# Optimization experiments

Measured on AMD Instinct MI355X. Metric: run time of the kernel, lower is better.

The kernel has to match this reference:

```python
import jax, jax.numpy as jnp
import numpy as np

B, N, L = 4, 64, 64
D_MODEL = 128
D_INNER = 256   # expand=2
D_STATE = 16
D_CONV = 4
DT_RANK = 8     # ceil(D_MODEL/16)
N_LAYERS = 4
EPS = 1e-5


def setup_inputs() -> dict:
    key = jax.random.key(0)
    ks = jax.random.split(key, 16)
    f = jnp.float32
    s = 0.05
    return {
        'mha_in': jax.random.normal(ks[0], (B, N, L, D_MODEL), f),
        'mamba_mask': jax.random.bernoulli(ks[1], 0.9, (B, N, L)),
        'mlp_w1': jax.random.normal(ks[2], (D_MODEL, D_MODEL), f) * s,
        'mlp_b1': jnp.zeros((D_MODEL,), f),
        'mlp_w2': jax.random.normal(ks[3], (D_MODEL, D_MODEL), f) * s,
        'mlp_b2': jnp.zeros((D_MODEL,), f),
        'in_proj_w': jax.random.normal(ks[4], (N_LAYERS, 2 * D_INNER, D_MODEL), f) * s,
        'conv_w': jax.random.normal(ks[5], (N_LAYERS, D_INNER, D_CONV), f) * s,
        'conv_b': jnp.zeros((N_LAYERS, D_INNER), f),
        'x_proj_w': jax.random.normal(ks[6], (N_LAYERS, DT_RANK + 2 * D_STATE, D_INNER), f) * s,
        'dt_proj_w': jax.random.normal(ks[7], (N_LAYERS, D_INNER, DT_RANK), f) * s,
        'dt_proj_b': jax.random.uniform(ks[8], (N_LAYERS, D_INNER), f, -4.0, -2.0),
        'A_log': jnp.log(jnp.broadcast_to(jnp.arange(1, D_STATE + 1, dtype=f), (N_LAYERS, D_INNER, D_STATE))),
        'D_skip': jnp.ones((N_LAYERS, D_INNER), f),
        'out_proj_w': jax.random.normal(ks[9], (N_LAYERS, D_MODEL, D_INNER), f) * s,
        'blk_norm_w': jnp.ones((N_LAYERS, D_MODEL), f),
        'norm_f_w': jnp.ones((D_MODEL,), f),
    }


def rmsnorm(x, w):
    # fused add-RMSNorm keeps residual in fp32; weight multiply after normalize
    x32 = x.astype(jnp.float32)
    return (x32 * jax.lax.rsqrt(jnp.mean(x32 * x32, -1, keepdims=True) + EPS)) * w


def causal_conv1d(x, w, b):
    # x: [R, L, d_inner]; depthwise causal conv (torch conv1d, padding=D_CONV-1, truncated to L)
    xp = jnp.pad(x, ((0, 0), (D_CONV - 1, 0), (0, 0)))
    y = jnp.zeros_like(x) + b
    for k in range(D_CONV):
        y = y + w[:, k] * xp[:, k:k + L, :]
    return y


def selective_scan(u, dt, A, Bm, Cm, D_sk):
    # u, dt: [R, L, d_inner]; A: [d_inner, n]; Bm, Cm: [R, L, n]
    def step(h, inputs):
        dt_t, B_t, C_t, u_t = inputs  # [R,di], [R,n], [R,n], [R,di]
        dA = jnp.exp(dt_t[..., None] * A)                       # [R,di,n]
        h = dA * h + (dt_t * u_t)[..., None] * B_t[:, None, :]  # [R,di,n]
        y = jnp.einsum('rdn,rn->rd', h, C_t)
        return h, y
    h0 = jnp.zeros((u.shape[0], A.shape[0], A.shape[1]), u.dtype)
    xs = (dt.swapaxes(0, 1), Bm.swapaxes(0, 1), Cm.swapaxes(0, 1), u.swapaxes(0, 1))
    _, ys = jax.lax.scan(step, h0, xs)
    return ys.swapaxes(0, 1) + u * D_sk


def mamba_mixer(x, in_w, conv_w, conv_b, xproj_w, dt_w, dt_b, A_log, D_sk, out_w):
    xz = x @ in_w.T                             # [R,L,2*d_inner]
    xc, z = jnp.split(xz, 2, axis=-1)
    xc = jax.nn.silu(causal_conv1d(xc, conv_w, conv_b))
    x_dbl = xc @ xproj_w.T                      # [R,L,dt_rank+2n]
    dt = jax.nn.softplus(x_dbl[..., :DT_RANK] @ dt_w.T + dt_b)
    Bm = x_dbl[..., DT_RANK:DT_RANK + D_STATE]
    Cm = x_dbl[..., DT_RANK + D_STATE:]
    A = -jnp.exp(A_log)
    y = selective_scan(xc, dt, A, Bm, Cm, D_sk)
    return (y * jax.nn.silu(z)) @ out_w.T


def _forward(mha_in, mamba_mask, mlp_w1, mlp_b1, mlp_w2, mlp_b2, in_proj_w, conv_w,
             conv_b, x_proj_w, dt_proj_w, dt_proj_b, A_log, D_skip, out_proj_w,
             blk_norm_w, norm_f_w):
    R = B * N
    x = mha_in.reshape(R, L, D_MODEL)
    key_valid = jnp.any(mamba_mask.reshape(R, L), axis=-1)
    # hist_embed_mlp: Linear -> GELU(exact) -> Linear
    h = jax.nn.gelu(x @ mlp_w1.T + mlp_b1, approximate=False) @ mlp_w2.T + mlp_b2
    residual = None
    for i in range(N_LAYERS):
        residual = h if residual is None else h + residual  # fused add (fp32 residual)
        hn = rmsnorm(residual, blk_norm_w[i])
        h = mamba_mixer(hn, in_proj_w[i], conv_w[i], conv_b[i], x_proj_w[i],
                        dt_proj_w[i], dt_proj_b[i], A_log[i], D_skip[i], out_proj_w[i])
    residual = h + residual
    out = rmsnorm(residual, norm_f_w)            # prenorm=False final fused add-norm
    # scatter into zeros over valid rows == mask-multiply (rows independent)
    out = out * key_valid[:, None, None].astype(out.dtype)
    out = out.reshape(B, N, L, D_MODEL)
    return out[:, 0, -1, :]                      # ag_feat[:, -1, :]


def reference(mha_in, mamba_mask, mlp_w1, mlp_b1, mlp_w2, mlp_b2, in_proj_w, conv_w,
              conv_b, x_proj_w, dt_proj_w, dt_proj_b, A_log, D_skip, out_proj_w,
              blk_norm_w, norm_f_w):
    return _forward(mha_in, mamba_mask, mlp_w1, mlp_b1, mlp_w2, mlp_b2, in_proj_w,
                    conv_w, conv_b, x_proj_w, dt_proj_w, dt_proj_b, A_log, D_skip,
                    out_proj_w, blk_norm_w, norm_f_w)
```

## Files before the change

kernel.cpp:

```cpp
#include <hip/hip_runtime.h>
#include <math.h>

#define NWG  64
#define NTHR 512

#define WS_XG 512
#define WS_DT (WS_XG + 65536)
#define WS_DU (WS_DT + 65536)
#define WS_BC (WS_DU + 65536)
#define WS_Y  (WS_BC + 8192)

__device__ __forceinline__ float silu_f(float v) { return v / (1.0f + __expf(-v)); }
__device__ __forceinline__ float dot4(float4 a, float4 b) {
    return a.x*b.x + a.y*b.y + a.z*b.z + a.w*b.w;
}
__device__ __forceinline__ float wave_red_sum(float v) {
    v += __shfl_xor(v, 1);  v += __shfl_xor(v, 2);  v += __shfl_xor(v, 4);
    v += __shfl_xor(v, 8);  v += __shfl_xor(v, 16); v += __shfl_xor(v, 32);
    return v;
}
__device__ __forceinline__ float red8(float v) {
    v += __shfl_xor(v, 1);  v += __shfl_xor(v, 2);  v += __shfl_xor(v, 4);
    return v;
}
__device__ __forceinline__ float sel4(int ln, float a0, float a1, float a2, float a3) {
    return ln==0 ? a0 : (ln==1 ? a1 : (ln==2 ? a2 : a3));
}
__device__ __forceinline__ float aload(const float* p) {
    return __hip_atomic_load(p, __ATOMIC_RELAXED, __HIP_MEMORY_SCOPE_AGENT);
}
__device__ __forceinline__ void astore(float* p, float v) {
    __hip_atomic_store(p, v, __ATOMIC_RELAXED, __HIP_MEMORY_SCOPE_AGENT);
}

__device__ __forceinline__ void seq_barrier(unsigned* slot) {
    __syncthreads();
    if (threadIdx.x == 0) {
        asm volatile("s_waitcnt vmcnt(0)" ::: "memory");
        __hip_atomic_fetch_add(slot, 1u, __ATOMIC_RELAXED, __HIP_MEMORY_SCOPE_AGENT);
        while (__hip_atomic_load(slot, __ATOMIC_RELAXED, __HIP_MEMORY_SCOPE_AGENT) < 16u)
            __builtin_amdgcn_s_sleep(1);
    }
    __syncthreads();
}

__global__ __launch_bounds__(NTHR, 1) void fused_kernel(
    const float* __restrict__ mha_in, const int* __restrict__ mask,
    const float* __restrict__ mlp_w1, const float* __restrict__ mlp_b1,
    const float* __restrict__ mlp_w2, const float* __restrict__ mlp_b2,
    const float* __restrict__ in_proj_w, const float* __restrict__ conv_w,
    const float* __restrict__ conv_b, const float* __restrict__ x_proj_w,
    const float* __restrict__ dt_proj_w, const float* __restrict__ dt_proj_b,
    const float* __restrict__ A_log, const float* __restrict__ D_skip,
    const float* __restrict__ out_proj_w, const float* __restrict__ blk_norm_w,
    const float* __restrict__ norm_f_w,
    float* __restrict__ ws, float* __restrict__ out)
{
    const int wg = blockIdx.x;
    const int t  = threadIdx.x;
    const int s  = wg & 3;
    const int rb = wg >> 2;
    const int l0 = rb * 4;
    const int r0 = s*64 + l0;
    const int d0 = rb * 16;
    const int h  = t >> 7;
    const int c  = t & 127;
    const int wave = t >> 6;
    const int grp = t >> 3, ln = t & 7;

    unsigned* bar = (unsigned*)ws;
    float* xg  = ws + WS_XG;
    float* dtg = ws + WS_DT;
    float* dug = ws + WS_DU;
    float* bcg = ws + WS_BC;
    float* yg  = ws + WS_Y;

    __shared__ float bufX[4][256];
    __shared__ float bufZ[4][256];
    __shared__ float bufA[4][256];
    __shared__ float bufG[4][256];
    __shared__ float bufB[4][128];
    __shared__ float bufR[4][128];
    __shared__ float xdS[4][40];
    __shared__ float sdt[64][17];
    __shared__ float sdu[64][17];
    __shared__ float sbc[64][33];
    __shared__ float part[8];
    __shared__ int   anyv;

    float resid;

    float4 w1v[8], w2v[8];
    {
        #pragma unroll
        for (int pass = 0; pass < 2; ++pass) {
            const int j = pass*64 + grp;
            const float* w1p = mlp_w1 + (size_t)j*128 + ln*4;
            const float* w2p = mlp_w2 + (size_t)j*128 + ln*4;
            #pragma unroll
            for (int i = 0; i < 4; ++i) {
                w1v[pass*4+i] = *(const float4*)&w1p[i*32];
                w2v[pass*4+i] = *(const float4*)&w2p[i*32];
            }
        }
    }
    bufB[h][c] = mha_in[(size_t)s*524288 + (size_t)(l0 + h)*128 + c];
    __syncthreads();
    {
        #pragma unroll
        for (int pass = 0; pass < 2; ++pass) {
            const int j = pass*64 + grp;
            float a0=0.f, a1=0.f, a2=0.f, a3=0.f;
            #pragma unroll
            for (int i = 0; i < 4; ++i) {
                float4 wv = w1v[pass*4+i];
                a0 += dot4(*(const float4*)&bufB[0][ln*4 + i*32], wv);
                a1 += dot4(*(const float4*)&bufB[1][ln*4 + i*32], wv);
                a2 += dot4(*(const float4*)&bufB[2][ln*4 + i*32], wv);
                a3 += dot4(*(const float4*)&bufB[3][ln*4 + i*32], wv);
            }
            a0 = red8(a0); a1 = red8(a1); a2 = red8(a2); a3 = red8(a3);
            if (ln < 4) {
                float v = sel4(ln, a0, a1, a2, a3) + mlp_b1[j];
                bufA[ln][j] = 0.5f*v*(1.0f + erff(v*0.70710678118f));
            }
        }
    }
    __syncthreads();
    {
        #pragma unroll
        for (int pass = 0; pass < 2; ++pass) {
            const int j = pass*64 + grp;
            float a0=0.f, a1=0.f, a2=0.f, a3=0.f;
            #pragma unroll
            for (int i = 0; i < 4; ++i) {
                float4 wv = w2v[pass*4+i];
                a0 += dot4(*(const float4*)&bufA[0][ln*4 + i*32], wv);
                a1 += dot4(*(const float4*)&bufA[1][ln*4 + i*32], wv);
                a2 += dot4(*(const float4*)&bufA[2][ln*4 + i*32], wv);
                a3 += dot4(*(const float4*)&bufA[3][ln*4 + i*32], wv);
            }
            a0 = red8(a0); a1 = red8(a1); a2 = red8(a2); a3 = red8(a3);
            if (ln < 4)
                bufR[ln][j] = sel4(ln, a0, a1, a2, a3) + mlp_b2[j];
        }
    }
    __syncthreads();
    resid = bufR[h][c];
    __syncthreads();

    for (int layer = 0; layer < 4; ++layer) {
        unsigned* s1slot = bar + (layer*4 + s)*16;
        unsigned* s2slot = bar + 256 + layer*4 + s;
        unsigned* s3slot = bar + 272 + layer*4 + s;

        float4 wx[16];
        {
            #pragma unroll
            for (int pass = 0; pass < 4; ++pass) {
                const float* w = in_proj_w + ((size_t)layer*512 + pass*64 + grp)*128 + ln*4;
                #pragma unroll
                for (int i = 0; i < 4; ++i) wx[pass*4+i] = *(const float4*)&w[i*32];
            }
        }

        {
            float sq = wave_red_sum(resid*resid);
            if ((t & 63) == 0) part[wave] = sq;
        }
        __syncthreads();
        {
            float sr = part[h*2] + part[h*2 + 1];
            float sc = rsqrtf(sr*(1.0f/128.0f) + 1e-5f);
            bufB[h][c] = resid * sc * blk_norm_w[layer*128 + c];
        }
        __syncthreads();

        {
            #pragma unroll
            for (int pass = 0; pass < 4; ++pass) {
                const int j = pass*64 + grp;
                float a0=0.f, a1=0.f, a2=0.f, a3=0.f;
                #pragma unroll
                for (int i = 0; i < 4; ++i) {
                    float4 wv = wx[pass*4+i];
                    a0 += dot4(*(const float4*)&bufB[0][ln*4 + i*32], wv);
                    a1 += dot4(*(const float4*)&bufB[1][ln*4 + i*32], wv);
                    a2 += dot4(*(const float4*)&bufB[2][ln*4 + i*32], wv);
                    a3 += dot4(*(const float4*)&bufB[3][ln*4 + i*32], wv);
                }
                a0 = red8(a0); a1 = red8(a1); a2 = red8(a2); a3 = red8(a3);
                if (ln < 4) {
                    float v = sel4(ln, a0, a1, a2, a3);
                    bufX[ln][j] = v;
                    astore(&xg[(size_t)(r0 + ln)*256 + j], v);
                }
            }
        }
        __syncthreads();
        if (t == 0) {
            asm volatile("s_waitcnt vmcnt(0)" ::: "memory");
            __hip_atomic_fetch_add(s1slot + rb, 1u, __ATOMIC_RELAXED, __HIP_MEMORY_SCOPE_AGENT);
            if (rb > 0) {
                while (__hip_atomic_load(s1slot + rb - 1, __ATOMIC_RELAXED, __HIP_MEMORY_SCOPE_AGENT) == 0u)
                    __builtin_amdgcn_s_sleep(1);
            }
        }
        __syncthreads();

        float4 wxp[8];
        if (t < 320) {
            const float* xw = x_proj_w + ((size_t)layer*40 + grp)*256 + ln*4;
            #pragma unroll
            for (int i = 0; i < 8; ++i) wxp[i] = *(const float4*)&xw[i*32];
        }

        {
            int d = t & 255, half = t >> 8;
            int rbase = s*64;
            float4 cw = *(const float4*)&conv_w[((size_t)layer*256 + d)*4];
            float cb = conv_b[layer*256 + d];
            if (half == 0) {
                float x0 = (l0-3 >= 0) ? aload(&xg[(size_t)(rbase+l0-3)*256 + d]) : 0.f;
                float x1 = (l0-2 >= 0) ? aload(&xg[(size_t)(rbase+l0-2)*256 + d]) : 0.f;
                float x2 = (l0-1 >= 0) ? aload(&xg[(size_t)(rbase+l0-1)*256 + d]) : 0.f;
                float x3 = bufX[0][d];
                float x4 = bufX[1][d];
                bufA[0][d] = silu_f(cb + cw.x*x0 + cw.y*x1 + cw.z*x2 + cw.w*x3);
                bufA[1][d] = silu_f(cb + cw.x*x1 + cw.y*x2 + cw.z*x3 + cw.w*x4);
            } else {
                float x0 = (l0-1 >= 0) ? aload(&xg[(size_t)(rbase+l0-1)*256 + d]) : 0.f;
                float x1 = bufX[0][d];
                float x2 = bufX[1][d];
                float x3 = bufX[2][d];
                float x4 = bufX[3][d];
                bufA[2][d] = silu_f(cb + cw.x*x0 + cw.y*x1 + cw.z*x2 + cw.w*x3);
                bufA[3][d] = silu_f(cb + cw.x*x1 + cw.y*x2 + cw.z*x3 + cw.w*x4);
            }
        }
        __syncthreads();

        if (t < 320) {
            const int jx = grp;
            float a0=0.f, a1=0.f, a2=0.f, a3=0.f;
            #pragma unroll
            for (int i = 0; i < 8; ++i) {
                float4 wv = wxp[i];
                a0 += dot4(*(const float4*)&bufA[0][ln*4 + i*32], wv);
                a1 += dot4(*(const float4*)&bufA[1][ln*4 + i*32], wv);
                a2 += dot4(*(const float4*)&bufA[2][ln*4 + i*32], wv);
                a3 += dot4(*(const float4*)&bufA[3][ln*4 + i*32], wv);
            }
            a0 = red8(a0); a1 = red8(a1); a2 = red8(a2); a3 = red8(a3);
            if (ln < 4) {
                float v = sel4(ln, a0, a1, a2, a3);
                xdS[ln][jx] = v;
                if (jx >= 8)
                    astore(&bcg[(size_t)(r0+ln)*32 + (jx-8)], v);
            }
        }
        __syncthreads();

        {
            int d = t & 255, half = t >> 8;
            const float* dw = dt_proj_w + ((size_t)layer*256 + d)*8;
            float4 wa = *(const float4*)&dw[0];
            float4 wb = *(const float4*)&dw[4];
            float b = dt_proj_b[layer*256 + d];
            #pragma unroll
            for (int q = 0; q < 2; ++q) {
                int rloc = half*2 + q;
                float4 xa = *(const float4*)&xdS[rloc][0];
                float4 xb = *(const float4*)&xdS[rloc][4];
                float pre = b + dot4(xa, wa) + dot4(xb, wb);
                float sp = (pre > 20.f) ? pre : log1pf(__expf(pre));
                astore(&dtg[(size_t)(r0+rloc)*256 + d], sp);
                astore(&dug[(size_t)(r0+rloc)*256 + d], sp * bufA[rloc][d]);
            }
        }
        seq_barrier(s2slot);

        if (t < 256) {
            int l = t >> 2, q = t & 3;
            const float* p = &dtg[(size_t)(s*64+l)*256 + d0 + q*4];
            sdt[l][q*4]   = aload(p);     sdt[l][q*4+1] = aload(p+1);
            sdt[l][q*4+2] = aload(p+2);   sdt[l][q*4+3] = aload(p+3);
        } else {
            int tt = t - 256; int l = tt >> 2, q = tt & 3;
            const float* p = &dug[(size_t)(s*64+l)*256 + d0 + q*4];
            sdu[l][q*4]   = aload(p);     sdu[l][q*4+1] = aload(p+1);
            sdu[l][q*4+2] = aload(p+2);   sdu[l][q*4+3] = aload(p+3);
        }
        {
            int l = t >> 3, q = t & 7;
            const float* p = &bcg[(size_t)(s*64+l)*32 + q*4];
            sbc[l][q*4]   = aload(p);     sbc[l][q*4+1] = aload(p+1);
            sbc[l][q*4+2] = aload(p+2);   sbc[l][q*4+3] = aload(p+3);
        }
        __syncthreads();

        if (t < 64) {
            const int dloc = t >> 2, sub = t & 3, d = d0 + dloc;
            const float* Ab = A_log + ((size_t)layer*256 + d)*16 + sub*4;
            float A0 = -__expf(Ab[0]), A1 = -__expf(Ab[1]);
            float A2 = -__expf(Ab[2]), A3 = -__expf(Ab[3]);
            float h0 = 0.f, h1v = 0.f, h2v = 0.f, h3v = 0.f;
            #pragma unroll 4
            for (int l = 0; l < 64; ++l) {
                float dtv = sdt[l][dloc];
                float duv = sdu[l][dloc];
                float4 B4, C4;
                B4.x = sbc[l][sub*4];      B4.y = sbc[l][sub*4+1];
                B4.z = sbc[l][sub*4+2];    B4.w = sbc[l][sub*4+3];
                C4.x = sbc[l][16+sub*4];   C4.y = sbc[l][16+sub*4+1];
                C4.z = sbc[l][16+sub*4+2]; C4.w = sbc[l][16+sub*4+3];
                float dA, yp;
                dA = __expf(dtv*A0); h0  = dA*h0  + duv*B4.x; yp  = h0 *C4.x;
                dA = __expf(dtv*A1); h1v = dA*h1v + duv*B4.y; yp += h1v*C4.y;
                dA = __expf(dtv*A2); h2v = dA*h2v + duv*B4.z; yp += h2v*C4.z;
                dA = __expf(dtv*A3); h3v = dA*h3v + duv*B4.w; yp += h3v*C4.w;
                yp += __shfl_xor(yp, 1);
                yp += __shfl_xor(yp, 2);
                if (sub == 0) astore(&yg[(size_t)(s*64+l)*256 + d], yp);
            }
        } else if (t >= 256) {
            const int tz = t - 256, gz = tz >> 3, lz = tz & 7;
            #pragma unroll
            for (int halfb = 0; halfb < 2; ++halfb) {
                float4 wv[16];
                #pragma unroll
                for (int pass = 0; pass < 4; ++pass) {
                    const int j = (halfb*4 + pass)*32 + gz;
                    const float* w = in_proj_w + ((size_t)layer*512 + 256 + j)*128 + lz*4;
                    #pragma unroll
                    for (int i = 0; i < 4; ++i) wv[pass*4+i] = *(const float4*)&w[i*32];
                }
                #pragma unroll
                for (int pass = 0; pass < 4; ++pass) {
                    const int j = (halfb*4 + pass)*32 + gz;
                    float a0=0.f, a1=0.f, a2=0.f, a3=0.f;
                    #pragma unroll
                    for (int i = 0; i < 4; ++i) {
                        float4 w4 = wv[pass*4+i];
                        a0 += dot4(*(const float4*)&bufB[0][lz*4 + i*32], w4);
                        a1 += dot4(*(const float4*)&bufB[1][lz*4 + i*32], w4);
                        a2 += dot4(*(const float4*)&bufB[2][lz*4 + i*32], w4);
                        a3 += dot4(*(const float4*)&bufB[3][lz*4 + i*32], w4);
                    }
                    a0 += __shfl_xor(a0, 1); a0 += __shfl_xor(a0, 2); a0 += __shfl_xor(a0, 4);
                    a1 += __shfl_xor(a1, 1); a1 += __shfl_xor(a1, 2); a1 += __shfl_xor(a1, 4);
                    a2 += __shfl_xor(a2, 1); a2 += __shfl_xor(a2, 2); a2 += __shfl_xor(a2, 4);
                    a3 += __shfl_xor(a3, 1); a3 += __shfl_xor(a3, 2); a3 += __shfl_xor(a3, 4);
                    if (lz < 4)
                        bufZ[lz][j] = sel4(lz, a0, a1, a2, a3);
                }
            }
        }
        seq_barrier(s3slot);

        float4 wo[16];
        {
            #pragma unroll
            for (int pass = 0; pass < 2; ++pass) {
                const float* w = out_proj_w + ((size_t)layer*128 + pass*64 + grp)*256 + ln*4;
                #pragma unroll
                for (int i = 0; i < 8; ++i) wo[pass*8+i] = *(const float4*)&w[i*32];
            }
        }

        {
            int d = t & 255, half = t >> 8;
            float Dsk = D_skip[layer*256 + d];
            #pragma unroll
            for (int q = 0; q < 2; ++q) {
                int rloc = half*2 + q; int r = r0 + rloc;
                float z = bufZ[rloc][d];
                float yv = aload(&yg[(size_t)r*256 + d]) + bufA[rloc][d]*Dsk;
                bufG[rloc][d] = yv * silu_f(z);
            }
        }
        __syncthreads();

        {
            #pragma unroll
            for (int pass = 0; pass < 2; ++pass) {
                const int j = pass*64 + grp;
                float a0=0.f, a1=0.f, a2=0.f, a3=0.f;
                #pragma unroll
                for (int i = 0; i < 8; ++i) {
                    float4 wv = wo[pass*8+i];
                    a0 += dot4(*(const float4*)&bufG[0][ln*4 + i*32], wv);
                    a1 += dot4(*(const float4*)&bufG[1][ln*4 + i*32], wv);
                    a2 += dot4(*(const float4*)&bufG[2][ln*4 + i*32], wv);
                    a3 += dot4(*(const float4*)&bufG[3][ln*4 + i*32], wv);
                }
                a0 = red8(a0); a1 = red8(a1); a2 = red8(a2); a3 = red8(a3);
                if (ln < 4)
                    bufR[ln][j] = sel4(ln, a0, a1, a2, a3);
            }
        }
        __syncthreads();
        resid += bufR[h][c];
        __syncthreads();
    }

    if (t == 0) anyv = 0;
    __syncthreads();
    if (rb == 15) {
        if (t < 64 && mask[s*4096 + t] != 0) anyv = 1;
        float sq = wave_red_sum(resid*resid);
        if ((t & 63) == 0) part[wave] = sq;
    }
    __syncthreads();
    if (rb == 15 && h == 3) {
        float sr = part[6] + part[7];
        float sc = rsqrtf(sr*(1.0f/128.0f) + 1e-5f);
        float o  = resid * sc * norm_f_w[c];
        out[s*128 + c] = anyv ? o : 0.f;
    }
}

extern "C" void kernel_launch(void* const* d_in, const int* in_sizes, int n_in,
                              void* d_out, int out_size, void* d_ws, size_t ws_size,
                              hipStream_t stream) {
    (void)in_sizes; (void)n_in; (void)out_size; (void)ws_size;
    const float* mha_in     = (const float*)d_in[0];
    const int*   mask       = (const int*)  d_in[1];
    const float* mlp_w1     = (const float*)d_in[2];
    const float* mlp_b1     = (const float*)d_in[3];
    const float* mlp_w2     = (const float*)d_in[4];
    const float* mlp_b2     = (const float*)d_in[5];
    const float* in_proj_w  = (const float*)d_in[6];
    const float* conv_w     = (const float*)d_in[7];
    const float* conv_b     = (const float*)d_in[8];
    const float* x_proj_w   = (const float*)d_in[9];
    const float* dt_proj_w  = (const float*)d_in[10];
    const float* dt_proj_b  = (const float*)d_in[11];
    const float* A_log      = (const float*)d_in[12];
    const float* D_skip     = (const float*)d_in[13];
    const float* out_proj_w = (const float*)d_in[14];
    const float* blk_norm_w = (const float*)d_in[15];
    const float* norm_f_w   = (const float*)d_in[16];
    float* ws  = (float*)d_ws;
    float* out = (float*)d_out;

    hipMemsetAsync(d_ws, 0, 2048, stream);

    fused_kernel<<<NWG, NTHR, 0, stream>>>(
        mha_in, mask, mlp_w1, mlp_b1, mlp_w2, mlp_b2,
        in_proj_w, conv_w, conv_b, x_proj_w, dt_proj_w, dt_proj_b,
        A_log, D_skip, out_proj_w, blk_norm_w, norm_f_w, ws, out);
}
```

Baseline: 205.2 us.

## Spread selective scan over four waves and prefetch next layer's in_proj weights

The selective scan now runs on 256 threads, one state element per lane, with a 16-lane shuffle reduction, instead of 64 threads each handling four states serially. This shortens the serial dependency chain of the scan recurrence. The next layer's in_proj weights are loaded into registers during the current layer's out_proj phase, so global load latency overlaps with compute. The cost is higher register pressure (a second 16-float4 buffer) and more shuffles per step.

```diff
diff --git a/kernel.cpp b/kernel.cpp
--- a/kernel.cpp
+++ b/kernel.cpp
@@ -149,20 +149,20 @@
     resid = bufR[h][c];
     __syncthreads();
 
+    float4 wx[16];
+    {
+        #pragma unroll
+        for (int pass = 0; pass < 4; ++pass) {
+            const float* w = in_proj_w + ((size_t)pass*64 + grp)*128 + ln*4;
+            #pragma unroll
+            for (int i = 0; i < 4; ++i) wx[pass*4+i] = *(const float4*)&w[i*32];
+        }
+    }
+
     for (int layer = 0; layer < 4; ++layer) {
         unsigned* s1slot = bar + (layer*4 + s)*16;
         unsigned* s2slot = bar + 256 + layer*4 + s;
         unsigned* s3slot = bar + 272 + layer*4 + s;
-
-        float4 wx[16];
-        {
-            #pragma unroll
-            for (int pass = 0; pass < 4; ++pass) {
-                const float* w = in_proj_w + ((size_t)layer*512 + pass*64 + grp)*128 + ln*4;
-                #pragma unroll
-                for (int i = 0; i < 4; ++i) wx[pass*4+i] = *(const float4*)&w[i*32];
-            }
-        }
 
         {
             float sq = wave_red_sum(resid*resid);
@@ -299,31 +299,29 @@
         }
         __syncthreads();
 
-        if (t < 64) {
-            const int dloc = t >> 2, sub = t & 3, d = d0 + dloc;
-            const float* Ab = A_log + ((size_t)layer*256 + d)*16 + sub*4;
-            float A0 = -__expf(Ab[0]), A1 = -__expf(Ab[1]);
-            float A2 = -__expf(Ab[2]), A3 = -__expf(Ab[3]);
-            float h0 = 0.f, h1v = 0.f, h2v = 0.f, h3v = 0.f;
+        if (t < 256) {
+            const int lane = t & 63, w4 = t >> 6;
+            const int cl = lane >> 4, n = lane & 15;
+            const int lch = w4*4 + cl;
+            const int d = d0 + lch;
+            const float A = -__expf(A_log[((size_t)(layer*256 + d))*16 + n]);
+            float hst = 0.f;
             #pragma unroll 4
             for (int l = 0; l < 64; ++l) {
-                float dtv = sdt[l][dloc];
-                float duv = sdu[l][dloc];
-                float4 B4, C4;
-                B4.x = sbc[l][sub*4];      B4.y = sbc[l][sub*4+1];
-                B4.z = sbc[l][sub*4+2];    B4.w = sbc[l][sub*4+3];
-                C4.x = sbc[l][16+sub*4];   C4.y = sbc[l][16+sub*4+1];
-                C4.z = sbc[l][16+sub*4+2]; C4.w = sbc[l][16+sub*4+3];
-                float dA, yp;
-                dA = __expf(dtv*A0); h0  = dA*h0  + duv*B4.x; yp  = h0 *C4.x;
-                dA = __expf(dtv*A1); h1v = dA*h1v + duv*B4.y; yp += h1v*C4.y;
-                dA = __expf(dtv*A2); h2v = dA*h2v + duv*B4.z; yp += h2v*C4.z;
-                dA = __expf(dtv*A3); h3v = dA*h3v + duv*B4.w; yp += h3v*C4.w;
-                yp += __shfl_xor(yp, 1);
-                yp += __shfl_xor(yp, 2);
-                if (sub == 0) astore(&yg[(size_t)(s*64+l)*256 + d], yp);
-            }
-        } else if (t >= 256) {
+                float dtv = sdt[l][lch];
+                float duv = sdu[l][lch];
+                float Bn  = sbc[l][n];
+                float Cn  = sbc[l][16 + n];
+                float dA  = __expf(dtv * A);
+                hst = dA*hst + duv*Bn;
+                float p = hst * Cn;
+                p += __shfl_xor(p, 1);
+                p += __shfl_xor(p, 2);
+                p += __shfl_xor(p, 4);
+                p += __shfl_xor(p, 8);
+                if (n == 0) astore(&yg[(size_t)(s*64+l)*256 + d], p);
+            }
+        } else {
             const int tz = t - 256, gz = tz >> 3, lz = tz & 7;
             #pragma unroll
             for (int halfb = 0; halfb < 2; ++halfb) {
@@ -367,6 +365,15 @@
                 for (int i = 0; i < 8; ++i) wo[pass*8+i] = *(const float4*)&w[i*32];
             }
         }
+        float4 wxn[16];
+        if (layer < 3) {
+            #pragma unroll
+            for (int pass = 0; pass < 4; ++pass) {
+                const float* w = in_proj_w + ((size_t)(layer+1)*512 + pass*64 + grp)*128 + ln*4;
+                #pragma unroll
+                for (int i = 0; i < 4; ++i) wxn[pass*4+i] = *(const float4*)&w[i*32];
+            }
+        }
 
         {
             int d = t & 255, half = t >> 8;
@@ -402,6 +409,11 @@
         __syncthreads();
         resid += bufR[h][c];
         __syncthreads();
+
+        if (layer < 3) {
+            #pragma unroll
+            for (int i = 0; i < 16; ++i) wx[i] = wxn[i];
+        }
     }
 
     if (t == 0) anyv = 0;
```

New measurement: 252.4 us. 23.0% more time.

## Halve workgroup count to 32 with 1024 threads, 8 rows per group

Applied to the files above, without the earlier changes.

Reworks the persistent fused kernel to launch 32 workgroups of 1024 threads instead of 64 of 512. Each group now owns 8 sequence positions and 32 scan channels, and all GEMV stages compute 8 rows per thread group with an 8-way select, so every reduction lane does useful work. The cross-workgroup barriers now wait for 8 arrivals instead of 16, which cuts inter-group synchronisation cost, but fewer compute units are used and registers per thread are tighter at 1024 threads.

```diff
diff --git a/kernel.cpp b/kernel.cpp
--- a/kernel.cpp
+++ b/kernel.cpp
@@ -1,8 +1,8 @@
 #include <hip/hip_runtime.h>
 #include <math.h>
 
-#define NWG  64
-#define NTHR 512
+#define NWG  32
+#define NTHR 1024
 
 #define WS_XG 512
 #define WS_DT (WS_XG + 65536)
@@ -23,8 +23,11 @@
     v += __shfl_xor(v, 1);  v += __shfl_xor(v, 2);  v += __shfl_xor(v, 4);
     return v;
 }
-__device__ __forceinline__ float sel4(int ln, float a0, float a1, float a2, float a3) {
-    return ln==0 ? a0 : (ln==1 ? a1 : (ln==2 ? a2 : a3));
+__device__ __forceinline__ float sel8(int ln, float a0, float a1, float a2, float a3,
+                                              float a4, float a5, float a6, float a7) {
+    float lo = ln==0 ? a0 : (ln==1 ? a1 : (ln==2 ? a2 : a3));
+    float hi = ln==4 ? a4 : (ln==5 ? a5 : (ln==6 ? a6 : a7));
+    return (ln < 4) ? lo : hi;
 }
 __device__ __forceinline__ float aload(const float* p) {
     return __hip_atomic_load(p, __ATOMIC_RELAXED, __HIP_MEMORY_SCOPE_AGENT);
@@ -38,7 +41,7 @@
     if (threadIdx.x == 0) {
         asm volatile("s_waitcnt vmcnt(0)" ::: "memory");
         __hip_atomic_fetch_add(slot, 1u, __ATOMIC_RELAXED, __HIP_MEMORY_SCOPE_AGENT);
-        while (__hip_atomic_load(slot, __ATOMIC_RELAXED, __HIP_MEMORY_SCOPE_AGENT) < 16u)
+        while (__hip_atomic_load(slot, __ATOMIC_RELAXED, __HIP_MEMORY_SCOPE_AGENT) < 8u)
             __builtin_amdgcn_s_sleep(1);
     }
     __syncthreads();
@@ -60,9 +63,9 @@
     const int t  = threadIdx.x;
     const int s  = wg & 3;
     const int rb = wg >> 2;
-    const int l0 = rb * 4;
+    const int l0 = rb * 8;
     const int r0 = s*64 + l0;
-    const int d0 = rb * 16;
+    const int d0 = rb * 32;
     const int h  = t >> 7;
     const int c  = t & 127;
     const int wave = t >> 6;
@@ -75,90 +78,87 @@
     float* bcg = ws + WS_BC;
     float* yg  = ws + WS_Y;
 
-    __shared__ float bufX[4][256];
-    __shared__ float bufZ[4][256];
-    __shared__ float bufA[4][256];
-    __shared__ float bufG[4][256];
-    __shared__ float bufB[4][128];
-    __shared__ float bufR[4][128];
-    __shared__ float xdS[4][40];
-    __shared__ float sdt[64][17];
-    __shared__ float sdu[64][17];
+    __shared__ float bufX[8][256];
+    __shared__ float bufZ[8][256];
+    __shared__ float bufA[8][256];
+    __shared__ float bufG[8][256];
+    __shared__ float bufB[8][128];
+    __shared__ float bufR[8][128];
+    __shared__ float xdS[8][40];
+    __shared__ float sdt[64][33];
+    __shared__ float sdu[64][33];
     __shared__ float sbc[64][33];
-    __shared__ float part[8];
+    __shared__ float part[16];
     __shared__ int   anyv;
 
     float resid;
 
-    float4 w1v[8], w2v[8];
+    float4 w1v[4], w2v[4];
     {
+        const float* w1p = mlp_w1 + (size_t)grp*128 + ln*4;
+        const float* w2p = mlp_w2 + (size_t)grp*128 + ln*4;
         #pragma unroll
-        for (int pass = 0; pass < 2; ++pass) {
-            const int j = pass*64 + grp;
-            const float* w1p = mlp_w1 + (size_t)j*128 + ln*4;
-            const float* w2p = mlp_w2 + (size_t)j*128 + ln*4;
-            #pragma unroll
-            for (int i = 0; i < 4; ++i) {
-                w1v[pass*4+i] = *(const float4*)&w1p[i*32];
-                w2v[pass*4+i] = *(const float4*)&w2p[i*32];
-            }
+        for (int i = 0; i < 4; ++i) {
+            w1v[i] = *(const float4*)&w1p[i*32];
+            w2v[i] = *(const float4*)&w2p[i*32];
         }
     }
     bufB[h][c] = mha_in[(size_t)s*524288 + (size_t)(l0 + h)*128 + c];
     __syncthreads();
     {
+        const int j = grp;
+        float a0=0.f,a1=0.f,a2=0.f,a3=0.f,a4=0.f,a5=0.f,a6=0.f,a7=0.f;
         #pragma unroll
-        for (int pass = 0; pass < 2; ++pass) {
-            const int j = pass*64 + grp;
-            float a0=0.f, a1=0.f, a2=0.f, a3=0.f;
-            #pragma unroll
-            for (int i = 0; i < 4; ++i) {
-                float4 wv = w1v[pass*4+i];
-                a0 += dot4(*(const float4*)&bufB[0][ln*4 + i*32], wv);
-                a1 += dot4(*(const float4*)&bufB[1][ln*4 + i*32], wv);
-                a2 += dot4(*(const float4*)&bufB[2][ln*4 + i*32], wv);
-                a3 += dot4(*(const float4*)&bufB[3][ln*4 + i*32], wv);
-            }
-            a0 = red8(a0); a1 = red8(a1); a2 = red8(a2); a3 = red8(a3);
-            if (ln < 4) {
-                float v = sel4(ln, a0, a1, a2, a3) + mlp_b1[j];
-                bufA[ln][j] = 0.5f*v*(1.0f + erff(v*0.70710678118f));
-            }
-        }
+        for (int i = 0; i < 4; ++i) {
+            float4 wv = w1v[i];
+            a0 += dot4(*(const float4*)&bufB[0][ln*4 + i*32], wv);
+            a1 += dot4(*(const float4*)&bufB[1][ln*4 + i*32], wv);
+            a2 += dot4(*(const float4*)&bufB[2][ln*4 + i*32], wv);
+            a3 += dot4(*(const float4*)&bufB[3][ln*4 + i*32], wv);
+            a4 += dot4(*(const float4*)&bufB[4][ln*4 + i*32], wv);
+            a5 += dot4(*(const float4*)&bufB[5][ln*4 + i*32], wv);
+            a6 += dot4(*(const float4*)&bufB[6][ln*4 + i*32], wv);
+            a7 += dot4(*(const float4*)&bufB[7][ln*4 + i*32], wv);
+        }
+        a0=red8(a0); a1=red8(a1); a2=red8(a2); a3=red8(a3);
+        a4=red8(a4); a5=red8(a5); a6=red8(a6); a7=red8(a7);
+        float v = sel8(ln, a0,a1,a2,a3,a4,a5,a6,a7) + mlp_b1[j];
+        bufA[ln][j] = 0.5f*v*(1.0f + erff(v*0.70710678118f));
     }
     __syncthreads();
     {
+        const int j = grp;
+        float a0=0.f,a1=0.f,a2=0.f,a3=0.f,a4=0.f,a5=0.f,a6=0.f,a7=0.f;
         #pragma unroll
-        for (int pass = 0; pass < 2; ++pass) {
-            const int j = pass*64 + grp;
-            float a0=0.f, a1=0.f, a2=0.f, a3=0.f;
-            #pragma unroll
-            for (int i = 0; i < 4; ++i) {
-                float4 wv = w2v[pass*4+i];
-                a0 += dot4(*(const float4*)&bufA[0][ln*4 + i*32], wv);
-                a1 += dot4(*(const float4*)&bufA[1][ln*4 + i*32], wv);
-                a2 += dot4(*(const float4*)&bufA[2][ln*4 + i*32], wv);
-                a3 += dot4(*(const float4*)&bufA[3][ln*4 + i*32], wv);
-            }
-            a0 = red8(a0); a1 = red8(a1); a2 = red8(a2); a3 = red8(a3);
-            if (ln < 4)
-                bufR[ln][j] = sel4(ln, a0, a1, a2, a3) + mlp_b2[j];
-        }
+        for (int i = 0; i < 4; ++i) {
+            float4 wv = w2v[i];
+            a0 += dot4(*(const float4*)&bufA[0][ln*4 + i*32], wv);
+            a1 += dot4(*(const float4*)&bufA[1][ln*4 + i*32], wv);
+            a2 += dot4(*(const float4*)&bufA[2][ln*4 + i*32], wv);
+            a3 += dot4(*(const float4*)&bufA[3][ln*4 + i*32], wv);
+            a4 += dot4(*(const float4*)&bufA[4][ln*4 + i*32], wv);
+            a5 += dot4(*(const float4*)&bufA[5][ln*4 + i*32], wv);
+            a6 += dot4(*(const float4*)&bufA[6][ln*4 + i*32], wv);
+            a7 += dot4(*(const float4*)&bufA[7][ln*4 + i*32], wv);
+        }
+        a0=red8(a0); a1=red8(a1); a2=red8(a2); a3=red8(a3);
+        a4=red8(a4); a5=red8(a5); a6=red8(a6); a7=red8(a7);
+        bufR[ln][j] = sel8(ln, a0,a1,a2,a3,a4,a5,a6,a7) + mlp_b2[j];
     }
     __syncthreads();
     resid = bufR[h][c];
     __syncthreads();
 
     for (int layer = 0; layer < 4; ++layer) {
-        unsigned* s1slot = bar + (layer*4 + s)*16;
+        unsigned* s1slot = bar + (layer*4 + s)*8;
         unsigned* s2slot = bar + 256 + layer*4 + s;
         unsigned* s3slot = bar + 272 + layer*4 + s;
 
-        float4 wx[16];
-        {
-            #pragma unroll
-            for (int pass = 0; pass < 4; ++pass) {
-                const float* w = in_proj_w + ((size_t)layer*512 + pass*64 + grp)*128 + ln*4;
+        float4 wx[8];
+        {
+            #pragma unroll
+            for (int pass = 0; pass < 2; ++pass) {
+                const float* w = in_proj_w + ((size_t)layer*512 + pass*128 + grp)*128 + ln*4;
                 #pragma unroll
                 for (int i = 0; i < 4; ++i) wx[pass*4+i] = *(const float4*)&w[i*32];
             }
@@ -178,9 +178,9 @@
 
         {
             #pragma unroll
-            for (int pass = 0; pass < 4; ++pass) {
-                const int j = pass*64 + grp;
-                float a0=0.f, a1=0.f, a2=0.f, a3=0.f;
+            for (int pass = 0; pass < 2; ++pass) {
+                const int j = pass*128 + grp;
+                float a0=0.f,a1=0.f,a2=0.f,a3=0.f,a4=0.f,a5=0.f,a6=0.f,a7=0.f;
                 #pragma unroll
                 for (int i = 0; i < 4; ++i) {
                     float4 wv = wx[pass*4+i];
@@ -188,13 +188,16 @@
                     a1 += dot4(*(const float4*)&bufB[1][ln*4 + i*32], wv);
                     a2 += dot4(*(const float4*)&bufB[2][ln*4 + i*32], wv);
                     a3 += dot4(*(const float4*)&bufB[3][ln*4 + i*32], wv);
+                    a4 += dot4(*(const float4*)&bufB[4][ln*4 + i*32], wv);
+                    a5 += dot4(*(const float4*)&bufB[5][ln*4 + i*32], wv);
+                    a6 += dot4(*(const float4*)&bufB[6][ln*4 + i*32], wv);
+                    a7 += dot4(*(const float4*)&bufB[7][ln*4 + i*32], wv);
                 }
-                a0 = red8(a0); a1 = red8(a1); a2 = red8(a2); a3 = red8(a3);
-                if (ln < 4) {
-                    float v = sel4(ln, a0, a1, a2, a3);
-                    bufX[ln][j] = v;
-                    astore(&xg[(size_t)(r0 + ln)*256 + j], v);
-                }
+                a0=red8(a0); a1=red8(a1); a2=red8(a2); a3=red8(a3);
+                a4=red8(a4); a5=red8(a5); a6=red8(a6); a7=red8(a7);
+                float v = sel8(ln, a0,a1,a2,a3,a4,a5,a6,a7);
+                bufX[ln][j] = v;
+                astore(&xg[(size_t)(r0 + ln)*256 + j], v);
             }
         }
         __syncthreads();
@@ -221,28 +224,41 @@
             float4 cw = *(const float4*)&conv_w[((size_t)layer*256 + d)*4];
             float cb = conv_b[layer*256 + d];
             if (half == 0) {
-                float x0 = (l0-3 >= 0) ? aload(&xg[(size_t)(rbase+l0-3)*256 + d]) : 0.f;
-                float x1 = (l0-2 >= 0) ? aload(&xg[(size_t)(rbase+l0-2)*256 + d]) : 0.f;
-                float x2 = (l0-1 >= 0) ? aload(&xg[(size_t)(rbase+l0-1)*256 + d]) : 0.f;
+                float x0 = 0.f, x1 = 0.f, x2 = 0.f;
+                if (rb > 0) {
+                    x0 = aload(&xg[(size_t)(rbase+l0-3)*256 + d]);
+                    x1 = aload(&xg[(size_t)(rbase+l0-2)*256 + d]);
+                    x2 = aload(&xg[(size_t)(rbase+l0-1)*256 + d]);
+                }
                 float x3 = bufX[0][d];
                 float x4 = bufX[1][d];
                 bufA[0][d] = silu_f(cb + cw.x*x0 + cw.y*x1 + cw.z*x2 + cw.w*x3);
                 bufA[1][d] = silu_f(cb + cw.x*x1 + cw.y*x2 + cw.z*x3 + cw.w*x4);
-            } else {
-                float x0 = (l0-1 >= 0) ? aload(&xg[(size_t)(rbase+l0-1)*256 + d]) : 0.f;
+            } else if (half == 1) {
+                float x0 = 0.f;
+                if (rb > 0) x0 = aload(&xg[(size_t)(rbase+l0-1)*256 + d]);
                 float x1 = bufX[0][d];
                 float x2 = bufX[1][d];
                 float x3 = bufX[2][d];
                 float x4 = bufX[3][d];
                 bufA[2][d] = silu_f(cb + cw.x*x0 + cw.y*x1 + cw.z*x2 + cw.w*x3);
                 bufA[3][d] = silu_f(cb + cw.x*x1 + cw.y*x2 + cw.z*x3 + cw.w*x4);
+            } else {
+                int m = half*2;
+                float x0 = bufX[m-3][d];
+                float x1 = bufX[m-2][d];
+                float x2 = bufX[m-1][d];
+                float x3 = bufX[m  ][d];
+                float x4 = bufX[m+1][d];
+                bufA[m  ][d] = silu_f(cb + cw.x*x0 + cw.y*x1 + cw.z*x2 + cw.w*x3);
+                bufA[m+1][d] = silu_f(cb + cw.x*x1 + cw.y*x2 + cw.z*x3 + cw.w*x4);
             }
         }
         __syncthreads();
 
         if (t < 320) {
             const int jx = grp;
-            float a0=0.f, a1=0.f, a2=0.f, a3=0.f;
+            float a0=0.f,a1=0.f,a2=0.f,a3=0.f,a4=0.f,a5=0.f,a6=0.f,a7=0.f;
             #pragma unroll
             for (int i = 0; i < 8; ++i) {
                 float4 wv = wxp[i];
@@ -250,14 +266,17 @@
                 a1 += dot4(*(const float4*)&bufA[1][ln*4 + i*32], wv);
                 a2 += dot4(*(const float4*)&bufA[2][ln*4 + i*32], wv);
                 a3 += dot4(*(const float4*)&bufA[3][ln*4 + i*32], wv);
-            }
-            a0 = red8(a0); a1 = red8(a1); a2 = red8(a2); a3 = red8(a3);
-            if (ln < 4) {
-                float v = sel4(ln, a0, a1, a2, a3);
-                xdS[ln][jx] = v;
-                if (jx >= 8)
-                    astore(&bcg[(size_t)(r0+ln)*32 + (jx-8)], v);
-            }
+                a4 += dot4(*(const float4*)&bufA[4][ln*4 + i*32], wv);
+                a5 += dot4(*(const float4*)&bufA[5][ln*4 + i*32], wv);
+                a6 += dot4(*(const float4*)&bufA[6][ln*4 + i*32], wv);
+                a7 += dot4(*(const float4*)&bufA[7][ln*4 + i*32], wv);
+            }
+            a0=red8(a0); a1=red8(a1); a2=red8(a2); a3=red8(a3);
+            a4=red8(a4); a5=red8(a5); a6=red8(a6); a7=red8(a7);
+            float v = sel8(ln, a0,a1,a2,a3,a4,a5,a6,a7);
+            xdS[ln][jx] = v;
+            if (jx >= 8)
+                astore(&bcg[(size_t)(r0+ln)*32 + (jx-8)], v);
         }
         __syncthreads();
 
@@ -280,26 +299,25 @@
         }
         seq_barrier(s2slot);
 
-        if (t < 256) {
-            int l = t >> 2, q = t & 3;
+        if (t < 512) {
+            int l = t >> 3, q = t & 7;
             const float* p = &dtg[(size_t)(s*64+l)*256 + d0 + q*4];
             sdt[l][q*4]   = aload(p);     sdt[l][q*4+1] = aload(p+1);
             sdt[l][q*4+2] = aload(p+2);   sdt[l][q*4+3] = aload(p+3);
         } else {
-            int tt = t - 256; int l = tt >> 2, q = tt & 3;
+            int tt = t - 512; int l = tt >> 3, q = tt & 7;
             const float* p = &dug[(size_t)(s*64+l)*256 + d0 + q*4];
             sdu[l][q*4]   = aload(p);     sdu[l][q*4+1] = aload(p+1);
             sdu[l][q*4+2] = aload(p+2);   sdu[l][q*4+3] = aload(p+3);
         }
         {
-            int l = t >> 3, q = t & 7;
-            const float* p = &bcg[(size_t)(s*64+l)*32 + q*4];
-            sbc[l][q*4]   = aload(p);     sbc[l][q*4+1] = aload(p+1);
-            sbc[l][q*4+2] = aload(p+2);   sbc[l][q*4+3] = aload(p+3);
-        }
-        __syncthreads();
-
-        if (t < 64) {
+            int l = t >> 4, q = t & 15;
+            const float* p = &bcg[(size_t)(s*64+l)*32 + q*2];
+            sbc[l][q*2]   = aload(p);     sbc[l][q*2+1] = aload(p+1);
+        }
+        __syncthreads();
+
+        if (t < 128) {
             const int dloc = t >> 2, sub = t & 3, d = d0 + dloc;
             const float* Ab = A_log + ((size_t)layer*256 + d)*16 + sub*4;
             float A0 = -__expf(Ab[0]), A1 = -__expf(Ab[1]);
@@ -323,22 +341,22 @@
                 yp += __shfl_xor(yp, 2);
                 if (sub == 0) astore(&yg[(size_t)(s*64+l)*256 + d], yp);
             }
-        } else if (t >= 256) {
-            const int tz = t - 256, gz = tz >> 3, lz = tz & 7;
+        } else if (t >= 512) {
+            const int tz = t - 512, gz = tz >> 3, lz = tz & 7;
             #pragma unroll
             for (int halfb = 0; halfb < 2; ++halfb) {
-                float4 wv[16];
+                float4 wv[8];
                 #pragma unroll
-                for (int pass = 0; pass < 4; ++pass) {
-                    const int j = (halfb*4 + pass)*32 + gz;
+                for (int pass = 0; pass < 2; ++pass) {
+                    const int j = (halfb*2 + pass)*64 + gz;
                     const float* w = in_proj_w + ((size_t)layer*512 + 256 + j)*128 + lz*4;
                     #pragma unroll
                     for (int i = 0; i < 4; ++i) wv[pass*4+i] = *(const float4*)&w[i*32];
                 }
                 #pragma unroll
-                for (int pass = 0; pass < 4; ++pass) {
-                    const int j = (halfb*4 + pass)*32 + gz;
-                    float a0=0.f, a1=0.f, a2=0.f, a3=0.f;
+                for (int pass = 0; pass < 2; ++pass) {
+                    const int j = (halfb*2 + pass)*64 + gz;
+                    float a0=0.f,a1=0.f,a2=0.f,a3=0.f,a4=0.f,a5=0.f,a6=0.f,a7=0.f;
                     #pragma unroll
                     for (int i = 0; i < 4; ++i) {
                         float4 w4 = wv[pass*4+i];
@@ -346,26 +364,24 @@
                         a1 += dot4(*(const float4*)&bufB[1][lz*4 + i*32], w4);
                         a2 += dot4(*(const float4*)&bufB[2][lz*4 + i*32], w4);
                         a3 += dot4(*(const float4*)&bufB[3][lz*4 + i*32], w4);
+                        a4 += dot4(*(const float4*)&bufB[4][lz*4 + i*32], w4);
+                        a5 += dot4(*(const float4*)&bufB[5][lz*4 + i*32], w4);
+                        a6 += dot4(*(const float4*)&bufB[6][lz*4 + i*32], w4);
+                        a7 += dot4(*(const float4*)&bufB[7][lz*4 + i*32], w4);
                     }
-                    a0 += __shfl_xor(a0, 1); a0 += __shfl_xor(a0, 2); a0 += __shfl_xor(a0, 4);
-                    a1 += __shfl_xor(a1, 1); a1 += __shfl_xor(a1, 2); a1 += __shfl_xor(a1, 4);
-                    a2 += __shfl_xor(a2, 1); a2 += __shfl_xor(a2, 2); a2 += __shfl_xor(a2, 4);
-                    a3 += __shfl_xor(a3, 1); a3 += __shfl_xor(a3, 2); a3 += __shfl_xor(a3, 4);
-                    if (lz < 4)
-                        bufZ[lz][j] = sel4(lz, a0, a1, a2, a3);
+                    a0=red8(a0); a1=red8(a1); a2=red8(a2); a3=red8(a3);
+                    a4=red8(a4); a5=red8(a5); a6=red8(a6); a7=red8(a7);
+                    bufZ[lz][j] = sel8(lz, a0,a1,a2,a3,a4,a5,a6,a7);
                 }
             }
         }
         seq_barrier(s3slot);
 
-        float4 wo[16];
-        {
-            #pragma unroll
-            for (int pass = 0; pass < 2; ++pass) {
-                const float* w = out_proj_w + ((size_t)layer*128 + pass*64 + grp)*256 + ln*4;
-                #pragma unroll
-                for (int i = 0; i < 8; ++i) wo[pass*8+i] = *(const float4*)&w[i*32];
-            }
+        float4 wo[8];
+        {
+            const float* w = out_proj_w + ((size_t)layer*128 + grp)*256 + ln*4;
+            #pragma unroll
+            for (int i = 0; i < 8; ++i) wo[i] = *(const float4*)&w[i*32];
         }
 
         {
@@ -382,22 +398,23 @@
         __syncthreads();
 
         {
-            #pragma unroll
-            for (int pass = 0; pass < 2; ++pass) {
-                const int j = pass*64 + grp;
-                float a0=0.f, a1=0.f, a2=0.f, a3=0.f;
-                #pragma unroll
-                for (int i = 0; i < 8; ++i) {
-                    float4 wv = wo[pass*8+i];
-                    a0 += dot4(*(const float4*)&bufG[0][ln*4 + i*32], wv);
-                    a1 += dot4(*(const float4*)&bufG[1][ln*4 + i*32], wv);
-                    a2 += dot4(*(const float4*)&bufG[2][ln*4 + i*32], wv);
-                    a3 += dot4(*(const float4*)&bufG[3][ln*4 + i*32], wv);
-                }
-                a0 = red8(a0); a1 = red8(a1); a2 = red8(a2); a3 = red8(a3);
-                if (ln < 4)
-                    bufR[ln][j] = sel4(ln, a0, a1, a2, a3);
-            }
+            const int j = grp;
+            float a0=0.f,a1=0.f,a2=0.f,a3=0.f,a4=0.f,a5=0.f,a6=0.f,a7=0.f;
+            #pragma unroll
+            for (int i = 0; i < 8; ++i) {
+                float4 wv = wo[i];
+                a0 += dot4(*(const float4*)&bufG[0][ln*4 + i*32], wv);
+                a1 += dot4(*(const float4*)&bufG[1][ln*4 + i*32], wv);
+                a2 += dot4(*(const float4*)&bufG[2][ln*4 + i*32], wv);
+                a3 += dot4(*(const float4*)&bufG[3][ln*4 + i*32], wv);
+                a4 += dot4(*(const float4*)&bufG[4][ln*4 + i*32], wv);
+                a5 += dot4(*(const float4*)&bufG[5][ln*4 + i*32], wv);
+                a6 += dot4(*(const float4*)&bufG[6][ln*4 + i*32], wv);
+                a7 += dot4(*(const float4*)&bufG[7][ln*4 + i*32], wv);
+            }
+            a0=red8(a0); a1=red8(a1); a2=red8(a2); a3=red8(a3);
+            a4=red8(a4); a5=red8(a5); a6=red8(a6); a7=red8(a7);
+            bufR[ln][j] = sel8(ln, a0,a1,a2,a3,a4,a5,a6,a7);
         }
         __syncthreads();
         resid += bufR[h][c];
@@ -406,14 +423,14 @@
 
     if (t == 0) anyv = 0;
     __syncthreads();
-    if (rb == 15) {
+    if (rb == 7) {
         if (t < 64 && mask[s*4096 + t] != 0) anyv = 1;
         float sq = wave_red_sum(resid*resid);
         if ((t & 63) == 0) part[wave] = sq;
     }
     __syncthreads();
-    if (rb == 15 && h == 3) {
-        float sr = part[6] + part[7];
+    if (rb == 7 && h == 7) {
+        float sr = part[14] + part[15];
         float sc = rsqrtf(sr*(1.0f/128.0f) + 1e-5f);
         float o  = resid * sc * norm_f_w[c];
         out[s*128 + c] = anyv ? o : 0.f;
```

Result: slower. 254.3 us (+23.9%).
